# Kernel tuning notes

Hardware: AMD Instinct MI355X
Metric: run time of the kernel (lower is better)

Reference implementation:

```python
import jax, jax.numpy as jnp
import numpy as np

PRIMES = np.array([2,3,5,7,11,13,17,19,23,29,31,37,41,43,47,53,59,61,67,71,73,79,83,89,97,101,103,107,109,113,127,131], dtype=np.float32)
ALPHA = 200.0       # sharpness of prime-divisibility gaussian
BETA = 2560.0       # sharpness of exponent-divisibility gaussian
MASK_POWER = 8      # crispness exponent on prime mask
TAU = 0.01          # torchsort soft_sort regularization_strength
MAX_K = 19          # floor(log2(2**20)); supports n < 2**20


def _isotonic_nonincreasing(y):
    """argmin_v ||v - y||^2 s.t. v_1 >= v_2 >= ... >= v_n.
    PAV solution via the min-max formula, fully vectorized (n is small: <= MAX_K)."""
    n = y.shape[0]
    z = -y
    big = jnp.asarray(jnp.finfo(z.dtype).max, z.dtype)
    cs = jnp.concatenate([jnp.zeros((1,), z.dtype), jnp.cumsum(z)])
    j = jnp.arange(n)[:, None]   # interval start
    k = jnp.arange(n)[None, :]   # interval end
    valid = k >= j
    den = jnp.where(valid, (k - j + 1).astype(z.dtype), jnp.ones((), z.dtype))
    means = jnp.where(valid, (cs[k + 1] - cs[j]) / den, big)  # mean(z[j..k])
    # suff[j,i] = min_{k >= i} means[j,k]
    suff = jnp.flip(jax.lax.cummin(jnp.flip(means, 1), axis=1), 1)
    i = jnp.arange(n)[None, :]
    A = jnp.where(j <= i, suff, -big)
    v = jnp.max(A, axis=0)  # v_i = max_{j<=i} min_{k>=i} mean(z[j..k])
    return -v


def _soft_sort_asc(x, tau):
    """torchsort.soft_sort (l2 regularization), ascending, 1-D input.
    out = -(w - isotonic_nonincreasing(w - s)), w = [n..1]/tau, s = desc-sort(-x)."""
    n = x.shape[0]
    w = jnp.arange(n, 0, -1, dtype=x.dtype) / tau
    s = -jnp.sort(x)[::-1]  # descending sort of -x
    sol = _isotonic_nonincreasing(w - s)
    return -(w - sol)


def _soft_exponents(n, primes, log_primes):
    """Soft exponent v_p(n) for all primes, vectorized over the prime axis."""
    ratios = n / primes                                   # [P]
    frac = ratios - jnp.round(ratios)
    mask_p = jnp.exp(-ALPHA * frac * frac) ** MASK_POWER
    mask_p = mask_p * (ratios / (ratios + (ratios == 0).astype(ratios.dtype)))
    max_k = jnp.floor(jnp.log(n) / log_primes)            # [P] data-dependent candidate count
    ks = jnp.arange(1, MAX_K + 1, dtype=primes.dtype)     # [K]
    r = n / (primes[:, None] ** ks[None, :])              # [P,K]
    fr = r - jnp.round(r)
    mk = jnp.exp(-BETA * fr * fr)
    # pad/mask instead of variable-length arange(1, max_k+1)
    scores = jnp.where(ks[None, :] <= max_k[:, None], mk * ks[None, :], jnp.zeros((), primes.dtype))
    sorted_scores = jax.vmap(_soft_sort_asc, in_axes=(0, None))(scores, TAU)  # [P,K] ascending
    k_hat = sorted_scores[:, -1]
    # gate: mask_p < 0.99 or max_k == 0 -> exponent 0 (no gradient, as in torch)
    return jnp.where((mask_p >= 0.99) & (max_k >= 1.0), k_hat, jnp.zeros((), primes.dtype))


def _forward(n1, n2, primes, log_primes):
    e1 = _soft_exponents(n1.reshape(()), primes, log_primes)
    e2 = _soft_exponents(n2.reshape(()), primes, log_primes)
    stacked = jnp.stack((e1, e2), axis=-1)                          # [P,2]
    sorted_pair = jax.vmap(_soft_sort_asc, in_axes=(0, None))(stacked, TAU)
    min_exp = sorted_pair[:, 0]
    return jnp.exp(jnp.sum(min_exp * log_primes))


def setup_inputs() -> dict:
    primes = jnp.asarray(PRIMES)
    return {
        "n1": jnp.asarray(720720.0, jnp.float32),  # 2^4*3^2*5*7*11*13
        "n2": jnp.asarray(831600.0, jnp.float32),  # 2^4*3^3*5^2*7*11
        "primes": primes,
        "log_primes": jnp.log(primes),
    }


def reference(n1, n2, primes, log_primes):
    return _forward(n1, n2, primes, log_primes)
```

## Files before the change

kernel.cpp:

```cpp
#include <hip/hip_runtime.h>
#include <math.h>

#define NPRIMES 32
#define MAXK    19
#define TAU     0.01f

#define MASK_C  (-2308.3120655f)
#define BETA_C  (-3693.2993047f)

__device__ __forceinline__ float soft_exponent(float n, float p, float lp) {
    float ratio  = n / p;
    float frac   = ratio - rintf(ratio);
    float mask_p = exp2f(MASK_C * frac * frac);
    float denom  = ratio + ((ratio == 0.0f) ? 1.0f : 0.0f);
    mask_p      *= ratio / denom;
    float max_k  = floorf(logf(n) / lp);

    float s[MAXK];
    float pk = 1.0f;
#pragma unroll
    for (int k = 1; k <= MAXK; ++k) {
        pk *= p;
        float r  = n / pk;
        float fr = r - rintf(r);
        float mk = exp2f(BETA_C * fr * fr);
        s[k - 1] = ((float)k <= max_k) ? mk * (float)k : 0.0f;
    }

#pragma unroll
    for (int r = 0; r < MAXK; ++r) {
#pragma unroll
        for (int i = (r & 1); i + 1 < MAXK; i += 2) {
            float a = s[i], b = s[i + 1];
            s[i]     = fmaxf(a, b);
            s[i + 1] = fminf(a, b);
        }
    }

    float cs = 0.0f, cs18 = 0.0f;
#pragma unroll
    for (int i = 0; i < MAXK; ++i) {
        if (i == MAXK - 1) cs18 = cs;
        float y = (float)(MAXK - i) / TAU + s[i];
        cs = cs - y;
    }
    float v     = cs - cs18;
    float k_hat = -v - (1.0f / TAU);

    return ((mask_p >= 0.99f) && (max_k >= 1.0f)) ? k_hat : 0.0f;
}

__global__ void softgcd_kernel(const float* __restrict__ n1p,
                               const float* __restrict__ n2p,
                               const float* __restrict__ primes,
                               const float* __restrict__ logp,
                               float* __restrict__ out) {
    const int lane  = threadIdx.x;
    const int pidx  = lane >> 1;
    const int which = lane & 1;

    const float p  = primes[pidx];
    const float lp = logp[pidx];
    const float n  = which ? n2p[0] : n1p[0];

    const float e  = soft_exponent(n, p, lp);
    const float ep = __shfl_xor(e, 1, 64);

    const float hi = fmaxf(e, ep);
    const float lo = fminf(e, ep);
    const float z0 = -(200.0f + hi);
    const float z1 = -(100.0f + lo);
    const float v0 = fminf(z0, (z0 + z1) * 0.5f);
    const float out0 = -v0 - 200.0f;

    float contrib = which ? 0.0f : out0 * lp;

    for (int off = 32; off > 0; off >>= 1)
        contrib += __shfl_down(contrib, off, 64);
    if (lane == 0)
        out[0] = expf(contrib);
}

extern "C" void kernel_launch(void* const* d_in, const int* in_sizes, int n_in,
                              void* d_out, int out_size, void* d_ws, size_t ws_size,
                              hipStream_t stream) {
    const float* n1     = (const float*)d_in[0];
    const float* n2     = (const float*)d_in[1];
    const float* primes = (const float*)d_in[2];
    const float* logp   = (const float*)d_in[3];
    float* out = (float*)d_out;
    softgcd_kernel<<<dim3(1), dim3(64), 0, stream>>>(n1, n2, primes, logp, out);
}
```

Measured before the change: 9.665 us.

## Replace soft-sort networks with closed-form min/max and threshold mask

The soft sort of each score vector is replaced by a running minimum, since with this tau the isotonic step reduces to the smallest score. The pairwise soft sort becomes a plain max of the two exponents, valid while their gap stays under the regularization scale. The exp2-based mask test is turned into a squared-fraction threshold, and the per-k divisions by p^k become repeated multiplication by an approximate reciprocal. This removes a 19-element sorting network and many divisions from a single-wave kernel. The cost is reliance on the tau scale and small rounding differences from the reciprocal chain.

```diff
diff --git a/kernel.cpp b/kernel.cpp
--- a/kernel.cpp
+++ b/kernel.cpp
@@ -3,51 +3,29 @@
 
 #define NPRIMES 32
 #define MAXK    19
-#define TAU     0.01f
+#define FLT_BIG 3.402823466e+38f
 
-#define MASK_C  (-2308.3120655f)
 #define BETA_C  (-3693.2993047f)
+#define MASK_THR 6.2815e-6f
 
 __device__ __forceinline__ float soft_exponent(float n, float p, float lp) {
-    float ratio  = n / p;
-    float frac   = ratio - rintf(ratio);
-    float mask_p = exp2f(MASK_C * frac * frac);
-    float denom  = ratio + ((ratio == 0.0f) ? 1.0f : 0.0f);
-    mask_p      *= ratio / denom;
+    float ratio = n / p;
+    float frac  = ratio - rintf(ratio);
+    bool  maskok = (frac * frac <= MASK_THR);
     float max_k  = floorf(logf(n) / lp);
 
-    float s[MAXK];
-    float pk = 1.0f;
+    float rp = __builtin_amdgcn_rcpf(p);
+    float r  = n;
+    float m  = FLT_BIG;
 #pragma unroll
     for (int k = 1; k <= MAXK; ++k) {
-        pk *= p;
-        float r  = n / pk;
+        r *= rp;
         float fr = r - rintf(r);
         float mk = exp2f(BETA_C * fr * fr);
-        s[k - 1] = ((float)k <= max_k) ? mk * (float)k : 0.0f;
+        float sc = ((float)k <= max_k) ? mk * (float)k : 0.0f;
+        m = fminf(m, sc);
     }
-
-#pragma unroll
-    for (int r = 0; r < MAXK; ++r) {
-#pragma unroll
-        for (int i = (r & 1); i + 1 < MAXK; i += 2) {
-            float a = s[i], b = s[i + 1];
-            s[i]     = fmaxf(a, b);
-            s[i + 1] = fminf(a, b);
-        }
-    }
-
-    float cs = 0.0f, cs18 = 0.0f;
-#pragma unroll
-    for (int i = 0; i < MAXK; ++i) {
-        if (i == MAXK - 1) cs18 = cs;
-        float y = (float)(MAXK - i) / TAU + s[i];
-        cs = cs - y;
-    }
-    float v     = cs - cs18;
-    float k_hat = -v - (1.0f / TAU);
-
-    return ((mask_p >= 0.99f) && (max_k >= 1.0f)) ? k_hat : 0.0f;
+    return (maskok && (max_k >= 1.0f)) ? m : 0.0f;
 }
 
 __global__ void softgcd_kernel(const float* __restrict__ n1p,
@@ -66,14 +44,7 @@
     const float e  = soft_exponent(n, p, lp);
     const float ep = __shfl_xor(e, 1, 64);
 
-    const float hi = fmaxf(e, ep);
-    const float lo = fminf(e, ep);
-    const float z0 = -(200.0f + hi);
-    const float z1 = -(100.0f + lo);
-    const float v0 = fminf(z0, (z0 + z1) * 0.5f);
-    const float out0 = -v0 - 200.0f;
-
-    float contrib = which ? 0.0f : out0 * lp;
+    float contrib = which ? 0.0f : fmaxf(e, ep) * lp;
 
     for (int off = 32; off > 0; off >>= 1)
         contrib += __shfl_down(contrib, off, 64);
```

Measured after the change: 9.757 us. No clear change (+0.9%).
